# Kernel tuning notes

Hardware: AMD Instinct MI355X
Metric: run time of the kernel (lower is better)

The kernel has to match this reference:

```python
import jax, jax.numpy as jnp
import numpy as np

B, H, W = 16, 32, 64
HID, VOCAB, ENC_C, EMB = 256, 5000, 1024, 256


def _conv3x3(x, w, b):
    # x: [B,C,H,W], w: [O,I,3,3]
    y = jax.lax.conv_general_dilated(x, w, (1, 1), 'SAME',
                                     dimension_numbers=('NCHW', 'OIHW', 'NCHW'))
    return y + b[None, :, None, None]


def _gru(x, h, w_ih, w_hh, b_ih, b_hh):
    # torch GRUCell: gates ordered r, z, n
    gi = x @ w_ih.T + b_ih
    gh = h @ w_hh.T + b_hh
    ir, iz, inn = jnp.split(gi, 3, axis=1)
    hr, hz, hn = jnp.split(gh, 3, axis=1)
    r = jax.nn.sigmoid(ir + hr)
    z = jax.nn.sigmoid(iz + hz)
    n = jnp.tanh(inn + r * hn)
    return (1.0 - z) * n + z * h


def setup_inputs() -> dict:
    key = jax.random.key(0)
    ks = jax.random.split(key, 48)
    g = lambda i, shape, s=0.02: jax.random.normal(ks[i], shape, jnp.float32) * s
    inp = {
        'input_a': jax.random.randint(ks[0], (B,), 0, VOCAB),
        'input_hidden': jax.random.normal(ks[1], (B, 1, HID), jnp.float32),
        'encoder_outputs': jax.random.normal(ks[2], (B, ENC_C, H, W), jnp.float32),
        'attention_sum': jnp.zeros((B, 1, H, W), jnp.float32),
        'decoder_attention': jnp.zeros((B, 1, H, W), jnp.float32),
        'h_mask': jax.random.randint(ks[3], (B,), 1, H + 1),
        'w_mask': jax.random.randint(ks[4], (B,), 1, W + 1),
        'feature_w': W, 'feature_h': H, 'batch_size': B, 'gpu': 0,
        # parameters
        'emb_w': g(5, (VOCAB, EMB)),
        'gru1_w_ih': g(6, (3 * HID, EMB)), 'gru1_w_hh': g(7, (3 * HID, HID)),
        'gru1_b_ih': jnp.zeros((3 * HID,)), 'gru1_b_hh': jnp.zeros((3 * HID,)),
        'fc1_w': g(8, (256, HID)), 'fc1_b': jnp.zeros((256,)),
        'gru2_w_ih': g(9, (3 * HID, ENC_C)), 'gru2_w_hh': g(10, (3 * HID, HID)),
        'gru2_b_ih': jnp.zeros((3 * HID,)), 'gru2_b_hh': jnp.zeros((3 * HID,)),
        'out_w': g(11, (VOCAB, 128)), 'out_b': jnp.zeros((VOCAB,)),
        'emb2_w': g(12, (128, 256)), 'emb2_b': jnp.zeros((128,)),
        'conv1_w': g(13, (1, 1, 3, 3)), 'conv1_b': jnp.zeros((1,)),
        'convtan_w': g(14, (256, 256, 3, 3)), 'convtan_b': jnp.zeros((256,)),
        'fc2_w': g(15, (128, HID)), 'fc2_b': jnp.zeros((128,)),
        'ua_w': g(16, (256, ENC_C)), 'ua_b': jnp.zeros((256,)),
        'uf_w': g(17, (256, 1)), 'uf_b': jnp.zeros((256,)),
        'v_w': g(18, (1, 256)), 'v_b': jnp.zeros((1,)),
        'wc_w': g(19, (128, ENC_C)), 'wc_b': jnp.zeros((128,)),
        'bn1_g': jnp.ones((256,)), 'bn1_b': jnp.zeros((256,)),
        'bn1_rm': jnp.zeros((256,)), 'bn1_rv': jnp.ones((256,)),
    }
    return inp


def reference(input_a, input_hidden, encoder_outputs, feature_w, attention_sum,
              decoder_attention, feature_h, batch_size, h_mask, w_mask, gpu,
              emb_w, gru1_w_ih, gru1_w_hh, gru1_b_ih, gru1_b_hh, fc1_w, fc1_b,
              gru2_w_ih, gru2_w_hh, gru2_b_ih, gru2_b_hh, out_w, out_b,
              emb2_w, emb2_b, conv1_w, conv1_b, convtan_w, convtan_b,
              fc2_w, fc2_b, ua_w, ua_b, uf_w, uf_b, v_w, v_b, wc_w, wc_b,
              bn1_g, bn1_b, bn1_rm, bn1_rv):
    # vectorized mask construction (replaces per-batch python loop)
    mask = ((jnp.arange(feature_h)[None, :, None] < h_mask[:, None, None]) &
            (jnp.arange(feature_w)[None, None, :] < w_mask[:, None, None])
            ).astype(jnp.float32)  # [B,H,W]

    emb = emb_w[input_a]                                   # [B,256] (dropout=eval id)
    h0 = input_hidden.reshape(batch_size, HID)
    st = _gru(emb, h0, gru1_w_ih, gru1_w_hh, gru1_b_ih, gru1_b_hh)  # [B,HID]
    hidden1 = (st @ fc1_w.T + fc1_b)[:, None, None, :]     # [B,1,1,256]

    enc_t = jnp.transpose(encoder_outputs, (0, 2, 3, 1))   # [B,H,W,1024]
    dec_att = _conv3x3(decoder_attention, conv1_w, conv1_b)
    att_sum = attention_sum + dec_att                      # [B,1,H,W]
    att_t = jnp.transpose(att_sum, (0, 2, 3, 1))           # [B,H,W,1]

    enc1 = enc_t @ ua_w.T + ua_b                           # [B,H,W,256]
    att1 = att_t @ uf_w.T + uf_b                           # [B,H,W,256]
    et = hidden1 + enc1 + att1

    et_c = jnp.transpose(et, (0, 3, 1, 2))                 # [B,256,H,W]
    et_c = _conv3x3(et_c, convtan_w, convtan_b)
    et_c = et_c * mask[:, None]
    inv_std = (bn1_g / jnp.sqrt(bn1_rv + 1e-5))[None, :, None, None]
    et_c = (et_c - bn1_rm[None, :, None, None]) * inv_std + bn1_b[None, :, None, None]
    et_c = jnp.tanh(et_c)
    et_hw = jnp.transpose(et_c, (0, 2, 3, 1))              # [B,H,W,256]

    e = (et_hw @ v_w.T + v_b)[..., 0]                      # [B,H,W]
    e_exp = jnp.exp(e) * mask
    e_sum = e_exp.sum((1, 2))                              # [B]
    alpha = e_exp / (e_sum[:, None, None] + 1e-8)
    alpha4 = alpha[:, None]                                # [B,1,H,W]

    ct = (alpha4 * encoder_outputs).sum((2, 3))            # [B,1024]
    h2 = _gru(ct, st, gru2_w_ih, gru2_w_hh, gru2_b_ih, gru2_b_hh)
    hidden_next = h2[:, None, :]                           # [B,1,HID]

    pre = (h2 @ fc2_w.T + fc2_b) + (emb @ emb2_w.T + emb2_b) + (ct @ wc_w.T + wc_b)
    output = jax.nn.log_softmax(pre @ out_w.T + out_b, axis=1)[:, None, :]  # [B,1,V]
    return (output, hidden_next, alpha4, att_sum)
```

## Files before the change

### kernel.cpp

```cpp
#include <hip/hip_runtime.h>
#include <hip/hip_bf16.h>

#define HH 32
#define WW 64
#define HWSZ 2048
#define ENC 1024
#define VOCAB 5000

typedef __attribute__((ext_vector_type(8))) short short8;
typedef __attribute__((ext_vector_type(4))) short short4v;
typedef __attribute__((ext_vector_type(4))) float f32x4;

#if defined(__has_builtin)
#if __has_builtin(__builtin_amdgcn_global_load_lds)
#define HAVE_GLD_LDS 1
#endif
#endif

__device__ __forceinline__ float sigm(float x) { return 1.0f / (1.0f + expf(-x)); }

__device__ __forceinline__ unsigned short f2bf(float x) {
    unsigned u = __float_as_uint(x);
    unsigned r = (u + 0x7fff + ((u >> 16) & 1)) >> 16;
    return (unsigned short)r;
}

#ifdef HAVE_GLD_LDS
__device__ __forceinline__ void gld_lds16(const unsigned short* g, unsigned short* l) {
    __builtin_amdgcn_global_load_lds(
        (const __attribute__((address_space(1))) void*)g,
        (__attribute__((address_space(3))) void*)l,
        16, 0, 0);
}
#endif

template <int NI>
__device__ __forceinline__ float dotk(const float* __restrict__ w,
                                      const float* __restrict__ x, int l) {
    float s = 0.f;
    #pragma unroll
    for (int i = 0; i < NI; ++i) {
        f32x4 wv = *(const f32x4*)(w + i * 64 + l * 4);
        f32x4 xv = *(const f32x4*)(x + i * 64 + l * 4);
        s += wv.x * xv.x + wv.y * xv.y + wv.z * xv.z + wv.w * xv.w;
    }
    return s;
}
__device__ __forceinline__ float red16(float s) {
    s += __shfl_xor(s, 1, 64);
    s += __shfl_xor(s, 2, 64);
    s += __shfl_xor(s, 4, 64);
    s += __shfl_xor(s, 8, 64);
    return s;
}

__global__ __launch_bounds__(256) void k_prep(
    const float* __restrict__ ua_w, unsigned short* __restrict__ ub,
    const float* __restrict__ cw, unsigned short* __restrict__ wr,
    const float* __restrict__ att_in, const float* __restrict__ dec,
    const float* __restrict__ c1w, const float* __restrict__ c1b,
    float* __restrict__ out_attsum,
    const float* __restrict__ wb, const float* __restrict__ g,
    const float* __restrict__ bb, const float* __restrict__ rm,
    const float* __restrict__ rv, float* __restrict__ cs, float* __restrict__ csh,
    const int* __restrict__ input_a, const float* __restrict__ input_hidden,
    const float* __restrict__ emb_w,
    const float* __restrict__ w_ih, const float* __restrict__ w_hh,
    const float* __restrict__ b_ih, const float* __restrict__ b_hh,
    float* __restrict__ gi, float* __restrict__ gh,
    float* __restrict__ e_zero)
{
    int blk = blockIdx.x, t = threadIdx.x;
    if (blk < 1024) {
        int idx = blk * 256 + t;
        ub[idx] = f2bf(ua_w[idx]);
    } else if (blk < 1280) {
        int idx = (blk - 1024) * 256 + t;
        const float* p = cw + (size_t)idx * 9;
        #pragma unroll
        for (int k = 0; k < 9; ++k) wr[k * 65536 + idx] = f2bf(p[k]);
    } else if (blk < 1408) {
        int idx = (blk - 1280) * 256 + t;
        int b = idx >> 11, hw = idx & 2047;
        int h = hw >> 6, w = hw & 63;
        float s = c1b[0];
        #pragma unroll
        for (int dy = 0; dy < 3; ++dy) {
            int hh = h + dy - 1;
            if ((unsigned)hh < (unsigned)HH) {
                #pragma unroll
                for (int dx = 0; dx < 3; ++dx) {
                    int wi = w + dx - 1;
                    if ((unsigned)wi < (unsigned)WW)
                        s += dec[b * HWSZ + hh * WW + wi] * c1w[dy * 3 + dx];
                }
            }
        }
        out_attsum[idx] = att_in[idx] + s;
    } else if (blk == 1408) {
        int c = t;
        float s = g[c] * rsqrtf(rv[c] + 1e-5f);
        cs[c] = s;
        csh[c] = (wb[c] - rm[c]) * s + bb[c];
    } else if (blk < 2177) {
        int gid = (blk - 1409) * 256 + t;
        int o = gid >> 4, l = gid & 15;
        int j = o >> 4, b = o & 15;
        int ia = input_a[b];
        float si = dotk<4>(w_ih + (size_t)j * 256, emb_w + (size_t)ia * 256, l);
        float sh = dotk<4>(w_hh + (size_t)j * 256, input_hidden + b * 256, l);
        si = red16(si); sh = red16(sh);
        if (l == 0) {
            gi[j * 16 + b] = si + b_ih[j];
            gh[j * 16 + b] = sh + b_hh[j];
        }
    } else {
        e_zero[(blk - 2177) * 256 + t] = 0.f;
    }
}

__global__ __launch_bounds__(256) void k_frontbc(
    const int* __restrict__ input_a, const float* __restrict__ emb_w,
    const float* __restrict__ input_hidden,
    const float* __restrict__ gi, const float* __restrict__ gh,
    const float* __restrict__ fc1_w, const float* __restrict__ fc1_b,
    const float* __restrict__ ua_b, const float* __restrict__ uf_b,
    float* __restrict__ st, float* __restrict__ embv, float* __restrict__ addc)
{
    __shared__ float st_s[256];
    int b = blockIdx.x, i = threadIdx.x;
    float r = sigm(gi[i * 16 + b] + gh[i * 16 + b]);
    float z = sigm(gi[(256 + i) * 16 + b] + gh[(256 + i) * 16 + b]);
    float n = tanhf(gi[(512 + i) * 16 + b] + r * gh[(512 + i) * 16 + b]);
    float h0 = input_hidden[b * 256 + i];
    float v = (1.f - z) * n + z * h0;
    st_s[i] = v;
    st[b * 256 + i] = v;
    embv[b * 256 + i] = emb_w[(size_t)input_a[b] * 256 + i];
    __syncthreads();
    int c = i;
    const float* w = fc1_w + (size_t)c * 256;
    float acc = 0.f;
    for (int k = 0; k < 256; ++k) acc += st_s[k] * w[k];
    addc[b * 256 + c] = acc + fc1_b[c] + ua_b[c] + uf_b[c];
}

__global__ __launch_bounds__(256) void k_et(
    const float* __restrict__ enc, const unsigned short* __restrict__ ua_bf,
    const float* __restrict__ addc, const float* __restrict__ uf_w,
    const float* __restrict__ attsum, unsigned short* __restrict__ et)
{
    __shared__ __align__(16) unsigned short As[256 * 64];
    __shared__ __align__(16) unsigned short Bs[32 * 64];
    int t = threadIdx.x;
    int hw0 = blockIdx.x * 32, b = blockIdx.y;
    int wv = t >> 6;
    int l15 = t & 15, quad = (t >> 4) & 3;
    int xb = l15 & 7;
    f32x4 acc[4][2];
    #pragma unroll
    for (int i = 0; i < 4; ++i)
        #pragma unroll
        for (int j = 0; j < 2; ++j) acc[i][j] = (f32x4)0.f;

    int p = t & 31, g3 = t >> 5;
    const float* encb = enc + (size_t)b * ENC * HWSZ + hw0 + p;

    float pfv[8];
    {
        const float* ep = encb + (size_t)(g3 * 8) * HWSZ;
        #pragma unroll
        for (int j = 0; j < 8; ++j) pfv[j] = ep[(size_t)j * HWSZ];
    }

    for (int k0 = 0; k0 < ENC; k0 += 64) {
        short8 bv;
        #pragma unroll
        for (int j = 0; j < 8; ++j) bv[j] = (short)f2bf(pfv[j]);
        if (k0 + 64 < ENC) {
            const float* ep = encb + (size_t)(k0 + 64 + g3 * 8) * HWSZ;
            #pragma unroll
            for (int j = 0; j < 8; ++j) pfv[j] = ep[(size_t)j * HWSZ];
        }
        __syncthreads();

        #pragma unroll
        for (int i = 0; i < 8; ++i) {
            int s = t + 256 * i;
            int c = s >> 3, kq = s & 7;
            const unsigned short* src =
                ua_bf + (size_t)c * ENC + k0 + ((kq ^ (c & 7)) << 3);
#ifdef HAVE_GLD_LDS
            gld_lds16(src, As + (size_t)(wv * 64 + 256 * i) * 8);
#else
            *(uint4*)(As + (size_t)s * 8) = *(const uint4*)src;
#endif
        }
        *(short8*)(Bs + p * 64 + ((g3 ^ (p & 7)) << 3)) = bv;
        __syncthreads();

        #pragma unroll
        for (int kk = 0; kk < 2; ++kk) {
            short8 af[4], bfr[2];
            #pragma unroll
            for (int mt = 0; mt < 4; ++mt) {
                int c = wv * 64 + mt * 16 + l15;
                af[mt] = *(const short8*)(As + c * 64 + (((kk * 4 + quad) ^ xb) << 3));
            }
            #pragma unroll
            for (int nt = 0; nt < 2; ++nt) {
                int n = nt * 16 + l15;
                bfr[nt] = *(const short8*)(Bs + n * 64 + (((kk * 4 + quad) ^ xb) << 3));
            }
            #pragma unroll
            for (int mt = 0; mt < 4; ++mt)
                #pragma unroll
                for (int nt = 0; nt < 2; ++nt)
                    acc[mt][nt] = __builtin_amdgcn_mfma_f32_16x16x32_bf16(
                        af[mt], bfr[nt], acc[mt][nt], 0, 0, 0);
        }
    }
    float at[2];
    #pragma unroll
    for (int nt = 0; nt < 2; ++nt) at[nt] = attsum[b * HWSZ + hw0 + nt * 16 + l15];
    #pragma unroll
    for (int mt = 0; mt < 4; ++mt) {
        int cb = wv * 64 + mt * 16 + quad * 4;
        float ad[4], uw[4];
        #pragma unroll
        for (int r = 0; r < 4; ++r) { ad[r] = addc[b * 256 + cb + r]; uw[r] = uf_w[cb + r]; }
        #pragma unroll
        for (int nt = 0; nt < 2; ++nt) {
            ushort4 pk;
            pk.x = f2bf(acc[mt][nt][0] + ad[0] + at[nt] * uw[0]);
            pk.y = f2bf(acc[mt][nt][1] + ad[1] + at[nt] * uw[1]);
            pk.z = f2bf(acc[mt][nt][2] + ad[2] + at[nt] * uw[2]);
            pk.w = f2bf(acc[mt][nt][3] + ad[3] + at[nt] * uw[3]);
            *(ushort4*)(et + (size_t)(b * HWSZ + hw0 + nt * 16 + l15) * 256 + cb) = pk;
        }
    }
}

__global__ __launch_bounds__(256, 2) void k_conv(
    const unsigned short* __restrict__ et, const unsigned short* __restrict__ wr,
    const float* __restrict__ cs, const float* __restrict__ csh,
    const float* __restrict__ v_w, float* __restrict__ e_out)
{
    __shared__ __align__(16) unsigned short Ls[2][66 * 264];
    __shared__ float red[64][17];
    int t = threadIdx.x;
    int h = blockIdx.x, b = blockIdx.y;
    int wv = t >> 6, l15 = t & 15, quad = (t >> 4) & 3;
    f32x4 acc[4][4];
    #pragma unroll
    for (int i = 0; i < 4; ++i)
        #pragma unroll
        for (int j = 0; j < 4; ++j) acc[i][j] = (f32x4)0.f;

    int ibase = (h == 0) ? 1 : 0;
    int ni = (h == 0 || h == HH - 1) ? 2 : 3;
    const unsigned short* etb = et + (size_t)b * HH * WW * 256;

    uint4 sreg[9];
    auto sload = [&](int dy) {
        const unsigned short* rowp = etb + (size_t)(h + dy - 1) * WW * 256;
        #pragma unroll
        for (int j = 0; j < 9; ++j) {
            int idx = t + 256 * j;
            uint4 v = make_uint4(0u, 0u, 0u, 0u);
            if (idx < 2112) {
                int p = idx >> 5, s = idx & 31;
                if (p > 0 && p < 65)
                    v = *(const uint4*)(rowp + (p - 1) * 256 + s * 8);
            }
            sreg[j] = v;
        }
    };
    auto swrite = [&](int bufsel) {
        #pragma unroll
        for (int j = 0; j < 9; ++j) {
            int idx = t + 256 * j;
            if (idx < 2112) {
                int p = idx >> 5, s = idx & 31;
                *(uint4*)(&Ls[bufsel][p * 264 + s * 8]) = sreg[j];
            }
        }
    };

    sload(ibase);
    swrite(0);
    __syncthreads();

    for (int i = 0; i < ni; ++i) {
        if (i + 1 < ni) sload(ibase + i + 1);
        __builtin_amdgcn_sched_barrier(0);
        int dy = ibase + i;
        const unsigned short* L = &Ls[i & 1][0];
        __builtin_amdgcn_s_setprio(1);
        #pragma unroll
        for (int dx = 0; dx < 3; ++dx) {
            const unsigned short* wrt = wr + (size_t)(dy * 3 + dx) * 65536;
            #pragma unroll
            for (int kc = 0; kc < 8; ++kc) {
                short8 af[4], bfr[4];
                #pragma unroll
                for (int mt = 0; mt < 4; ++mt)
                    af[mt] = *(const short8*)(wrt +
                        (size_t)(wv * 64 + mt * 16 + l15) * 256 + kc * 32 + quad * 8);
                #pragma unroll
                for (int nt = 0; nt < 4; ++nt) {
                    int wrow = nt * 16 + l15 + dx;
                    bfr[nt] = *(const short8*)(L + wrow * 264 + kc * 32 + quad * 8);
                }
                #pragma unroll
                for (int mt = 0; mt < 4; ++mt)
                    #pragma unroll
                    for (int nt = 0; nt < 4; ++nt)
                        acc[mt][nt] = __builtin_amdgcn_mfma_f32_16x16x32_bf16(
                            af[mt], bfr[nt], acc[mt][nt], 0, 0, 0);
            }
        }
        __builtin_amdgcn_s_setprio(0);
        if (i + 1 < ni) swrite((i + 1) & 1);
        __syncthreads();
    }

    float p[4] = {0.f, 0.f, 0.f, 0.f};
    #pragma unroll
    for (int mt = 0; mt < 4; ++mt) {
        int cb = wv * 64 + mt * 16 + quad * 4;
        #pragma unroll
        for (int r = 0; r < 4; ++r) {
            float sc = cs[cb + r], sh = csh[cb + r], vw = v_w[cb + r];
            #pragma unroll
            for (int nt = 0; nt < 4; ++nt) {
                float x = acc[mt][nt][r] * sc + sh;
                p[nt] += tanhf(x) * vw;
            }
        }
    }
    #pragma unroll
    for (int nt = 0; nt < 4; ++nt) red[nt * 16 + l15][wv * 4 + quad] = p[nt];
    __syncthreads();
    if (t < 64) {
        float s = 0.f;
        #pragma unroll
        for (int i = 0; i < 16; ++i) s += red[t][i];
        e_out[(b * HH + h) * WW + t] = s;
    }
}

__global__ __launch_bounds__(256) void k_ctalpha(
    const float* __restrict__ enc, const float* __restrict__ e_acc,
    const float* __restrict__ v_b,
    const int* __restrict__ h_mask, const int* __restrict__ w_mask,
    float* __restrict__ alpha_out, float* __restrict__ ct)
{
    __shared__ float a_s[HWSZ];
    __shared__ float rbuf[4];
    int b = blockIdx.y, cg = blockIdx.x, t = threadIdx.x;
    int hm = h_mask[b], wm = w_mask[b];
    float vb = v_b[0];
    float vals[8];
    float psum = 0.f;
    #pragma unroll
    for (int u = 0; u < 8; ++u) {
        int s = u * 256 + t;
        int h = s >> 6, w = s & 63;
        float e = e_acc[b * HWSZ + s] + vb;
        float ex = (h < hm && w < wm) ? expf(e) : 0.f;
        vals[u] = ex;
        psum += ex;
    }
    for (int off = 1; off < 64; off <<= 1) psum += __shfl_xor(psum, off, 64);
    if ((t & 63) == 0) rbuf[t >> 6] = psum;
    __syncthreads();
    float inv = 1.f / (rbuf[0] + rbuf[1] + rbuf[2] + rbuf[3] + 1e-8f);
    #pragma unroll
    for (int u = 0; u < 8; ++u) {
        int s = u * 256 + t;
        float a = vals[u] * inv;
        a_s[s] = a;
        if (cg == 0) alpha_out[b * HWSZ + s] = a;
    }
    __syncthreads();
    int wave = t >> 6, lane = t & 63;
    int c = cg * 4 + wave;
    const float* ep = enc + ((size_t)(b * ENC + c)) * HWSZ;
    float s = 0.f;
    for (int i = lane; i < HWSZ; i += 64) s += ep[i] * a_s[i];
    for (int off = 32; off; off >>= 1) s += __shfl_down(s, off, 64);
    if (lane == 0) ct[b * ENC + c] = s;
}

__global__ __launch_bounds__(256) void k_gru2a(
    const float* __restrict__ ct, const float* __restrict__ st,
    const float* __restrict__ w_ih, const float* __restrict__ w_hh,
    const float* __restrict__ b_ih, const float* __restrict__ b_hh,
    float* __restrict__ gi, float* __restrict__ gh)
{
    int gid = blockIdx.x * 256 + threadIdx.x;
    int o = gid >> 4, l = gid & 15;
    int j = o >> 4, b = o & 15;
    float si = dotk<16>(w_ih + (size_t)j * ENC, ct + b * ENC, l);
    float sh = dotk<4>(w_hh + (size_t)j * 256, st + b * 256, l);
    si = red16(si); sh = red16(sh);
    if (l == 0) {
        gi[j * 16 + b] = si + b_ih[j];
        gh[j * 16 + b] = sh + b_hh[j];
    }
}

__global__ __launch_bounds__(256) void k_gates2(
    const float* __restrict__ st, const float* __restrict__ gi,
    const float* __restrict__ gh, float* __restrict__ h2,
    float* __restrict__ out_hidden)
{
    int b = blockIdx.x, i = threadIdx.x;
    float r = sigm(gi[i * 16 + b] + gh[i * 16 + b]);
    float z = sigm(gi[(256 + i) * 16 + b] + gh[(256 + i) * 16 + b]);
    float n = tanhf(gi[(512 + i) * 16 + b] + r * gh[(512 + i) * 16 + b]);
    float v = (1.f - z) * n + z * st[b * 256 + i];
    h2[b * 256 + i] = v;
    out_hidden[b * 256 + i] = v;
}

__global__ __launch_bounds__(256) void k_pre(
    const float* __restrict__ h2, const float* __restrict__ emb,
    const float* __restrict__ ct,
    const float* __restrict__ fc2_w, const float* __restrict__ fc2_b,
    const float* __restrict__ emb2_w, const float* __restrict__ emb2_b,
    const float* __restrict__ wc_w, const float* __restrict__ wc_b,
    float* __restrict__ pre)
{
    int gid = blockIdx.x * 256 + threadIdx.x;
    int o = gid >> 4, l = gid & 15;
    int j = o >> 4, b = o & 15;
    float s = dotk<4>(fc2_w + (size_t)j * 256, h2 + b * 256, l)
            + dotk<4>(emb2_w + (size_t)j * 256, emb + b * 256, l)
            + dotk<16>(wc_w + (size_t)j * ENC, ct + b * ENC, l);
    s = red16(s);
    if (l == 0) pre[b * 128 + j] = s + fc2_b[j] + emb2_b[j] + wc_b[j];
}

__global__ __launch_bounds__(256) void k_logits(
    const float* __restrict__ pre, const float* __restrict__ out_w,
    const float* __restrict__ out_b, float* __restrict__ logits)
{
    int gid = blockIdx.x * 256 + threadIdx.x;
    int o = gid >> 4, l = gid & 15;
    int j = o >> 4, b = o & 15;
    float s = dotk<2>(out_w + (size_t)j * 128, pre + b * 128, l);
    s = red16(s);
    if (l == 0) logits[b * VOCAB + j] = s + out_b[j];
}

__global__ __launch_bounds__(256) void k_lsm(
    const float* __restrict__ logits, float* __restrict__ out)
{
    __shared__ float buf[VOCAB];
    __shared__ float rbuf[4];
    int b = blockIdx.x, t = threadIdx.x;
    float mx = -1e30f;
    for (int s = t; s < VOCAB; s += 256) {
        float v = logits[b * VOCAB + s];
        buf[s] = v;
        mx = fmaxf(mx, v);
    }
    for (int off = 1; off < 64; off <<= 1) mx = fmaxf(mx, __shfl_xor(mx, off, 64));
    if ((t & 63) == 0) rbuf[t >> 6] = mx;
    __syncthreads();
    mx = fmaxf(fmaxf(rbuf[0], rbuf[1]), fmaxf(rbuf[2], rbuf[3]));
    __syncthreads();
    float se = 0.f;
    for (int s = t; s < VOCAB; s += 256) se += expf(buf[s] - mx);
    for (int off = 1; off < 64; off <<= 1) se += __shfl_xor(se, off, 64);
    if ((t & 63) == 0) rbuf[t >> 6] = se;
    __syncthreads();
    float lse = mx + logf(rbuf[0] + rbuf[1] + rbuf[2] + rbuf[3]);
    for (int s = t; s < VOCAB; s += 256) out[b * VOCAB + s] = buf[s] - lse;
}

extern "C" void kernel_launch(void* const* d_in, const int* in_sizes, int n_in,
                              void* d_out, int out_size, void* d_ws, size_t ws_size,
                              hipStream_t stream)
{
    const int*   input_a      = (const int*)d_in[0];
    const float* input_hidden = (const float*)d_in[1];
    const float* enc          = (const float*)d_in[2];
    const float* att_in       = (const float*)d_in[3];
    const float* dec_att      = (const float*)d_in[4];
    const int*   h_mask       = (const int*)d_in[5];
    const int*   w_mask       = (const int*)d_in[6];
    const float* emb_w        = (const float*)d_in[11];
    const float* g1_wih       = (const float*)d_in[12];
    const float* g1_whh       = (const float*)d_in[13];
    const float* g1_bih       = (const float*)d_in[14];
    const float* g1_bhh       = (const float*)d_in[15];
    const float* fc1_w        = (const float*)d_in[16];
    const float* fc1_b        = (const float*)d_in[17];
    const float* g2_wih       = (const float*)d_in[18];
    const float* g2_whh       = (const float*)d_in[19];
    const float* g2_bih       = (const float*)d_in[20];
    const float* g2_bhh       = (const float*)d_in[21];
    const float* out_w        = (const float*)d_in[22];
    const float* out_b        = (const float*)d_in[23];
    const float* emb2_w       = (const float*)d_in[24];
    const float* emb2_b       = (const float*)d_in[25];
    const float* c1w          = (const float*)d_in[26];
    const float* c1b          = (const float*)d_in[27];
    const float* ctw          = (const float*)d_in[28];
    const float* ctb          = (const float*)d_in[29];
    const float* fc2_w        = (const float*)d_in[30];
    const float* fc2_b        = (const float*)d_in[31];
    const float* ua_w         = (const float*)d_in[32];
    const float* ua_b         = (const float*)d_in[33];
    const float* uf_w         = (const float*)d_in[34];
    const float* uf_b         = (const float*)d_in[35];
    const float* v_w          = (const float*)d_in[36];
    const float* v_b          = (const float*)d_in[37];
    const float* wc_w         = (const float*)d_in[38];
    const float* wc_b         = (const float*)d_in[39];
    const float* bn_g         = (const float*)d_in[40];
    const float* bn_b         = (const float*)d_in[41];
    const float* bn_rm        = (const float*)d_in[42];
    const float* bn_rv        = (const float*)d_in[43];

    float* out        = (float*)d_out;
    float* out_logits = out;
    float* out_hidden = out + 80000;
    float* out_alpha  = out + 84096;
    float* out_attsum = out + 116864;

    char* ws = (char*)d_ws;
    unsigned short* et_t  = (unsigned short*)ws;
    unsigned short* ua_bf = (unsigned short*)(ws + 16777216);
    unsigned short* w_r   = (unsigned short*)(ws + 17301504);
    float* f      = (float*)(ws + 18481152);
    float* st     = f;
    float* embv   = f + 4096;
    float* addc   = f + 8192;
    float* e_ws   = f + 12288;
    float* ct     = f + 45056;
    float* h2     = f + 61440;
    float* pre    = f + 65536;
    float* logits = f + 67584;
    float* gi1    = f + 147584;
    float* gh1    = f + 159872;
    float* gi2    = f + 172160;
    float* gh2    = f + 184448;
    float* cs     = f + 196736;
    float* csh    = f + 196992;

    k_prep<<<2305, 256, 0, stream>>>(ua_w, ua_bf, ctw, w_r,
                                     att_in, dec_att, c1w, c1b, out_attsum,
                                     ctb, bn_g, bn_b, bn_rm, bn_rv, cs, csh,
                                     input_a, input_hidden, emb_w,
                                     g1_wih, g1_whh, g1_bih, g1_bhh, gi1, gh1,
                                     e_ws);
    k_frontbc<<<16, 256, 0, stream>>>(input_a, emb_w, input_hidden, gi1, gh1,
                                      fc1_w, fc1_b, ua_b, uf_b, st, embv, addc);

    k_et<<<dim3(64, 16), 256, 0, stream>>>(enc, ua_bf, addc, uf_w, out_attsum, et_t);
    k_conv<<<dim3(32, 16), 256, 0, stream>>>(et_t, w_r, cs, csh, v_w, e_ws);

    k_ctalpha<<<dim3(256, 16), 256, 0, stream>>>(enc, e_ws, v_b, h_mask, w_mask,
                                                 out_alpha, ct);
    k_gru2a<<<768, 256, 0, stream>>>(ct, st, g2_wih, g2_whh, g2_bih, g2_bhh, gi2, gh2);
    k_gates2<<<16, 256, 0, stream>>>(st, gi2, gh2, h2, out_hidden);
    k_pre<<<128, 256, 0, stream>>>(h2, embv, ct, fc2_w, fc2_b, emb2_w, emb2_b,
                                   wc_w, wc_b, pre);
    k_logits<<<5000, 256, 0, stream>>>(pre, out_w, out_b, logits);
    k_lsm<<<16, 256, 0, stream>>>(logits, out_logits);
}
```

Before: 459.7 us.

## Process two batches per conv block with direct-to-LDS swizzled staging

Each k_conv block now computes the 3x3 conv for two batch images at once. Every weight fragment loaded from global memory feeds MFMAs for both images, which halves weight traffic per output. Activation rows are staged with global_load_lds into an XOR-swizzled, unpadded LDS layout instead of going through registers into a padded layout. The grid halves to 256 blocks with launch bounds of one block per CU, so occupancy and latency hiding drop while accumulator register pressure doubles.

```diff
diff --git a/kernel.cpp b/kernel.cpp
--- a/kernel.cpp
+++ b/kernel.cpp
@@ -241,112 +241,124 @@
     }
 }
 
-__global__ __launch_bounds__(256, 2) void k_conv(
+__global__ __launch_bounds__(256, 1) void k_conv(
     const unsigned short* __restrict__ et, const unsigned short* __restrict__ wr,
     const float* __restrict__ cs, const float* __restrict__ csh,
     const float* __restrict__ v_w, float* __restrict__ e_out)
 {
-    __shared__ __align__(16) unsigned short Ls[2][66 * 264];
-    __shared__ float red[64][17];
+    __shared__ __align__(16) unsigned short Ls[2][2][66 * 256];
+    __shared__ float red[2][64][17];
     int t = threadIdx.x;
-    int h = blockIdx.x, b = blockIdx.y;
+    int h = blockIdx.x, b0 = blockIdx.y * 2;
     int wv = t >> 6, l15 = t & 15, quad = (t >> 4) & 3;
-    f32x4 acc[4][4];
-    #pragma unroll
-    for (int i = 0; i < 4; ++i)
-        #pragma unroll
-        for (int j = 0; j < 4; ++j) acc[i][j] = (f32x4)0.f;
+    f32x4 acc[2][4][4];
+    #pragma unroll
+    for (int bb = 0; bb < 2; ++bb)
+        #pragma unroll
+        for (int i = 0; i < 4; ++i)
+            #pragma unroll
+            for (int j = 0; j < 4; ++j) acc[bb][i][j] = (f32x4)0.f;
+
+    {
+        int rg = t >> 5, g = t & 31;
+        int buf = rg & 1, bb = (rg >> 1) & 1, rsel = rg >> 2;
+        *(short8*)(&Ls[buf][bb][(rsel ? 65 : 0) * 256 + g * 8]) = (short8)0;
+    }
 
     int ibase = (h == 0) ? 1 : 0;
     int ni = (h == 0 || h == HH - 1) ? 2 : 3;
-    const unsigned short* etb = et + (size_t)b * HH * WW * 256;
-
-    uint4 sreg[9];
-    auto sload = [&](int dy) {
-        const unsigned short* rowp = etb + (size_t)(h + dy - 1) * WW * 256;
-        #pragma unroll
-        for (int j = 0; j < 9; ++j) {
-            int idx = t + 256 * j;
-            uint4 v = make_uint4(0u, 0u, 0u, 0u);
-            if (idx < 2112) {
-                int p = idx >> 5, s = idx & 31;
-                if (p > 0 && p < 65)
-                    v = *(const uint4*)(rowp + (p - 1) * 256 + s * 8);
-            }
-            sreg[j] = v;
+
+    auto stage = [&](int dy, int buf) {
+        int hr = h + dy - 1;
+        #pragma unroll
+        for (int j = 0; j < 16; ++j) {
+            int slot = t + 256 * j;
+            int bb = slot >> 11;
+            int rem = slot & 2047;
+            int px = rem >> 5, g = rem & 31;
+            const unsigned short* src = et
+                + ((size_t)(b0 + bb) * HH + hr) * (WW * 256)
+                + px * 256 + ((g ^ ((px + 1) & 7)) << 3);
+            int base = wv * 64 + 256 * j;
+            unsigned short* dst = &Ls[buf][base >> 11][256 + (base & 2047) * 8];
+#ifdef HAVE_GLD_LDS
+            gld_lds16(src, dst);
+#else
+            *(uint4*)(&Ls[buf][bb][256 + rem * 8]) = *(const uint4*)src;
+#endif
         }
     };
-    auto swrite = [&](int bufsel) {
-        #pragma unroll
-        for (int j = 0; j < 9; ++j) {
-            int idx = t + 256 * j;
-            if (idx < 2112) {
-                int p = idx >> 5, s = idx & 31;
-                *(uint4*)(&Ls[bufsel][p * 264 + s * 8]) = sreg[j];
-            }
-        }
-    };
-
-    sload(ibase);
-    swrite(0);
+
+    stage(ibase, 0);
     __syncthreads();
 
     for (int i = 0; i < ni; ++i) {
-        if (i + 1 < ni) sload(ibase + i + 1);
+        if (i + 1 < ni) stage(ibase + i + 1, (i + 1) & 1);
         __builtin_amdgcn_sched_barrier(0);
         int dy = ibase + i;
-        const unsigned short* L = &Ls[i & 1][0];
-        __builtin_amdgcn_s_setprio(1);
+        const unsigned short* L0 = &Ls[i & 1][0][0];
+        const unsigned short* L1 = &Ls[i & 1][1][0];
         #pragma unroll
         for (int dx = 0; dx < 3; ++dx) {
             const unsigned short* wrt = wr + (size_t)(dy * 3 + dx) * 65536;
             #pragma unroll
             for (int kc = 0; kc < 8; ++kc) {
-                short8 af[4], bfr[4];
+                short8 af[4], b0f[4], b1f[4];
                 #pragma unroll
                 for (int mt = 0; mt < 4; ++mt)
                     af[mt] = *(const short8*)(wrt +
                         (size_t)(wv * 64 + mt * 16 + l15) * 256 + kc * 32 + quad * 8);
+                int g0 = kc * 4 + quad;
                 #pragma unroll
                 for (int nt = 0; nt < 4; ++nt) {
                     int wrow = nt * 16 + l15 + dx;
-                    bfr[nt] = *(const short8*)(L + wrow * 264 + kc * 32 + quad * 8);
+                    int gr = g0 ^ (wrow & 7);
+                    b0f[nt] = *(const short8*)(L0 + wrow * 256 + gr * 8);
+                    b1f[nt] = *(const short8*)(L1 + wrow * 256 + gr * 8);
                 }
                 #pragma unroll
                 for (int mt = 0; mt < 4; ++mt)
                     #pragma unroll
-                    for (int nt = 0; nt < 4; ++nt)
-                        acc[mt][nt] = __builtin_amdgcn_mfma_f32_16x16x32_bf16(
-                            af[mt], bfr[nt], acc[mt][nt], 0, 0, 0);
+                    for (int nt = 0; nt < 4; ++nt) {
+                        acc[0][mt][nt] = __builtin_amdgcn_mfma_f32_16x16x32_bf16(
+                            af[mt], b0f[nt], acc[0][mt][nt], 0, 0, 0);
+                        acc[1][mt][nt] = __builtin_amdgcn_mfma_f32_16x16x32_bf16(
+                            af[mt], b1f[nt], acc[1][mt][nt], 0, 0, 0);
+                    }
             }
         }
-        __builtin_amdgcn_s_setprio(0);
-        if (i + 1 < ni) swrite((i + 1) & 1);
         __syncthreads();
     }
 
-    float p[4] = {0.f, 0.f, 0.f, 0.f};
+    float pp[2][4] = {{0.f, 0.f, 0.f, 0.f}, {0.f, 0.f, 0.f, 0.f}};
     #pragma unroll
     for (int mt = 0; mt < 4; ++mt) {
         int cb = wv * 64 + mt * 16 + quad * 4;
         #pragma unroll
         for (int r = 0; r < 4; ++r) {
-            float sc = cs[cb + r], sh = csh[cb + r], vw = v_w[cb + r];
+            float sc = cs[cb + r], sh = csh[cb + r], vwv = v_w[cb + r];
             #pragma unroll
             for (int nt = 0; nt < 4; ++nt) {
-                float x = acc[mt][nt][r] * sc + sh;
-                p[nt] += tanhf(x) * vw;
+                #pragma unroll
+                for (int bb = 0; bb < 2; ++bb) {
+                    float x = acc[bb][mt][nt][r] * sc + sh;
+                    pp[bb][nt] += tanhf(x) * vwv;
+                }
             }
         }
     }
     #pragma unroll
-    for (int nt = 0; nt < 4; ++nt) red[nt * 16 + l15][wv * 4 + quad] = p[nt];
-    __syncthreads();
-    if (t < 64) {
+    for (int nt = 0; nt < 4; ++nt) {
+        red[0][nt * 16 + l15][wv * 4 + quad] = pp[0][nt];
+        red[1][nt * 16 + l15][wv * 4 + quad] = pp[1][nt];
+    }
+    __syncthreads();
+    if (t < 128) {
+        int bb = t >> 6, w = t & 63;
         float s = 0.f;
         #pragma unroll
-        for (int i = 0; i < 16; ++i) s += red[t][i];
-        e_out[(b * HH + h) * WW + t] = s;
+        for (int i = 0; i < 16; ++i) s += red[bb][w][i];
+        e_out[((b0 + bb) * HH + h) * WW + w] = s;
     }
 }
 
@@ -562,7 +574,7 @@
                                       fc1_w, fc1_b, ua_b, uf_b, st, embv, addc);
 
     k_et<<<dim3(64, 16), 256, 0, stream>>>(enc, ua_bf, addc, uf_w, out_attsum, et_t);
-    k_conv<<<dim3(32, 16), 256, 0, stream>>>(et_t, w_r, cs, csh, v_w, e_ws);
+    k_conv<<<dim3(32, 8), 256, 0, stream>>>(et_t, w_r, cs, csh, v_w, e_ws);
 
     k_ctalpha<<<dim3(256, 16), 256, 0, stream>>>(enc, e_ws, v_b, h_mask, w_mask,
                                                  out_alpha, ct);
```

Result: faster. 440.6 us (-4.2%).

## Single-buffer XOR-swizzled LDS tile in conv kernel, drop register prefetch

Applied to the files above, without the earlier changes.

Replaces the double-buffered, padded (264-stride) LDS row buffer with a single 256-stride buffer that uses an XOR swizzle on 16-byte groups to avoid bank conflicts. Zero-padding rows are written once up front instead of being loaded per iteration, and the register prefetch of the next input row overlapped with MFMA is removed in favour of load/sync/store/sync per row. This cuts LDS footprint, which may allow more occupancy, and simplifies addressing, but gives up overlap of global loads with compute.

```diff
diff --git a/kernel.cpp b/kernel.cpp
--- a/kernel.cpp
+++ b/kernel.cpp
@@ -246,7 +246,7 @@
     const float* __restrict__ cs, const float* __restrict__ csh,
     const float* __restrict__ v_w, float* __restrict__ e_out)
 {
-    __shared__ __align__(16) unsigned short Ls[2][66 * 264];
+    __shared__ __align__(16) unsigned short Ls[66 * 256];
     __shared__ float red[64][17];
     int t = threadIdx.x;
     int h = blockIdx.x, b = blockIdx.y;
@@ -257,45 +257,32 @@
         #pragma unroll
         for (int j = 0; j < 4; ++j) acc[i][j] = (f32x4)0.f;
 
+    if (t < 64) {
+        int rsel = t >> 5, g = t & 31;
+        *(short8*)(&Ls[(rsel ? 65 : 0) * 256 + g * 8]) = (short8)0;
+    }
+
     int ibase = (h == 0) ? 1 : 0;
     int ni = (h == 0 || h == HH - 1) ? 2 : 3;
     const unsigned short* etb = et + (size_t)b * HH * WW * 256;
 
-    uint4 sreg[9];
-    auto sload = [&](int dy) {
+    for (int i = 0; i < ni; ++i) {
+        int dy = ibase + i;
         const unsigned short* rowp = etb + (size_t)(h + dy - 1) * WW * 256;
-        #pragma unroll
-        for (int j = 0; j < 9; ++j) {
+        uint4 sv[8];
+        #pragma unroll
+        for (int j = 0; j < 8; ++j) {
             int idx = t + 256 * j;
-            uint4 v = make_uint4(0u, 0u, 0u, 0u);
-            if (idx < 2112) {
-                int p = idx >> 5, s = idx & 31;
-                if (p > 0 && p < 65)
-                    v = *(const uint4*)(rowp + (p - 1) * 256 + s * 8);
-            }
-            sreg[j] = v;
-        }
-    };
-    auto swrite = [&](int bufsel) {
-        #pragma unroll
-        for (int j = 0; j < 9; ++j) {
+            sv[j] = *(const uint4*)(rowp + (idx >> 5) * 256 + (idx & 31) * 8);
+        }
+        __syncthreads();
+        #pragma unroll
+        for (int j = 0; j < 8; ++j) {
             int idx = t + 256 * j;
-            if (idx < 2112) {
-                int p = idx >> 5, s = idx & 31;
-                *(uint4*)(&Ls[bufsel][p * 264 + s * 8]) = sreg[j];
-            }
-        }
-    };
-
-    sload(ibase);
-    swrite(0);
-    __syncthreads();
-
-    for (int i = 0; i < ni; ++i) {
-        if (i + 1 < ni) sload(ibase + i + 1);
-        __builtin_amdgcn_sched_barrier(0);
-        int dy = ibase + i;
-        const unsigned short* L = &Ls[i & 1][0];
+            int row = (idx >> 5) + 1, s = idx & 31;
+            *(uint4*)(&Ls[row * 256 + ((s ^ (row & 7)) << 3)]) = sv[j];
+        }
+        __syncthreads();
         __builtin_amdgcn_s_setprio(1);
         #pragma unroll
         for (int dx = 0; dx < 3; ++dx) {
@@ -307,10 +294,11 @@
                 for (int mt = 0; mt < 4; ++mt)
                     af[mt] = *(const short8*)(wrt +
                         (size_t)(wv * 64 + mt * 16 + l15) * 256 + kc * 32 + quad * 8);
+                int g0 = kc * 4 + quad;
                 #pragma unroll
                 for (int nt = 0; nt < 4; ++nt) {
-                    int wrow = nt * 16 + l15 + dx;
-                    bfr[nt] = *(const short8*)(L + wrow * 264 + kc * 32 + quad * 8);
+                    int row = nt * 16 + l15 + dx;
+                    bfr[nt] = *(const short8*)(&Ls[row * 256 + ((g0 ^ (row & 7)) << 3)]);
                 }
                 #pragma unroll
                 for (int mt = 0; mt < 4; ++mt)
@@ -321,8 +309,6 @@
             }
         }
         __builtin_amdgcn_s_setprio(0);
-        if (i + 1 < ni) swrite((i + 1) & 1);
-        __syncthreads();
     }
 
     float p[4] = {0.f, 0.f, 0.f, 0.f};
@@ -331,14 +317,15 @@
         int cb = wv * 64 + mt * 16 + quad * 4;
         #pragma unroll
         for (int r = 0; r < 4; ++r) {
-            float sc = cs[cb + r], sh = csh[cb + r], vw = v_w[cb + r];
+            float sc = cs[cb + r], sh = csh[cb + r], vwv = v_w[cb + r];
             #pragma unroll
             for (int nt = 0; nt < 4; ++nt) {
                 float x = acc[mt][nt][r] * sc + sh;
-                p[nt] += tanhf(x) * vw;
+                p[nt] += tanhf(x) * vwv;
             }
         }
     }
+    __syncthreads();
     #pragma unroll
     for (int nt = 0; nt < 4; ++nt) red[nt * 16 + l15][wv * 4 + quad] = p[nt];
     __syncthreads();
```

Measured after the change: 475.3 us. +3.4%, slower.
